# Kernel optimization log

Hardware: AMD Instinct MI355X
Metric: run time of the kernel (lower is better)

Reference implementation:

```python
import jax, jax.numpy as jnp
import numpy as np

D, H, F, E, K = 1024, 16, 2048, 8, 2
EPS = 1e-5


def layernorm(x, g, b):
    m = jnp.mean(x, axis=-1, keepdims=True)
    v = jnp.mean((x - m) ** 2, axis=-1, keepdims=True)
    return (x - m) * jax.lax.rsqrt(v + EPS) * g + b


def mha(q_in, k_in, v_in, wq, wk, wv, bq, bk, bv, wo, bo):
    B, Tq, Dm = q_in.shape
    Tk = k_in.shape[1]
    dh = Dm // H
    q = (q_in @ wq + bq).reshape(B, Tq, H, dh)
    k = (k_in @ wk + bk).reshape(B, Tk, H, dh)
    v = (v_in @ wv + bv).reshape(B, Tk, H, dh)
    scores = jnp.einsum('bqhd,bkhd->bhqk', q, k) / jnp.sqrt(jnp.asarray(dh, q.dtype))
    attn = jax.nn.softmax(scores, axis=-1)
    out = jnp.einsum('bhqk,bkhd->bqhd', attn, v).reshape(B, Tq, Dm)
    return out @ wo + bo


def moe(x, rw, rb, w1, b1, w2, b2):
    B, T, Dm = x.shape
    xt = x.reshape(-1, Dm)                      # [N, D]
    N = xt.shape[0]
    logits = xt @ rw + rb                       # [N, E]
    probs = jax.nn.softmax(logits, axis=-1)
    topv, topi = jax.lax.top_k(probs, K)        # [N, K]
    gates = topv / jnp.sum(topv, axis=-1, keepdims=True)
    dense_gates = jnp.zeros((N, E), x.dtype).at[jnp.arange(N)[:, None], topi].set(gates)
    h = jax.nn.relu(jnp.einsum('td,edf->etf', xt, w1) + b1[:, None, :])  # [E, N, F]
    y = jnp.einsum('etf,efd->etd', h, w2) + b2[:, None, :]               # [E, N, D]
    out = jnp.einsum('te,etd->td', dense_gates, y).reshape(B, T, Dm)
    frac = jnp.mean(jnp.sum(jax.nn.one_hot(topi, E, dtype=x.dtype), axis=1) / K, axis=0)  # [E]
    importance = jnp.mean(probs, axis=0)        # [E]
    lb_loss = E * jnp.sum(frac * importance)
    return out, lb_loss


def forward(tgt, memory,
            sa_wq, sa_wk, sa_wv, sa_bq, sa_bk, sa_bv, sa_wo, sa_bo,
            ca_wq, ca_wk, ca_wv, ca_bq, ca_bk, ca_bv, ca_wo, ca_bo,
            ln1_g, ln1_b, ln2_g, ln2_b, ln3_g, ln3_b,
            rw, rb, w1, b1, w2, b2):
    t2 = mha(tgt, tgt, tgt, sa_wq, sa_wk, sa_wv, sa_bq, sa_bk, sa_bv, sa_wo, sa_bo)
    t = layernorm(tgt + t2, ln1_g, ln1_b)
    t2 = mha(t, memory, memory, ca_wq, ca_wk, ca_wv, ca_bq, ca_bk, ca_bv, ca_wo, ca_bo)
    t = layernorm(t + t2, ln2_g, ln2_b)
    t2, lb = moe(t, rw, rb, w1, b1, w2, b2)
    t = layernorm(t + t2, ln3_g, ln3_b)
    return t, lb


def setup_inputs() -> dict:
    key = jax.random.key(0)
    ks = jax.random.split(key, 24)
    s = 1.0 / np.sqrt(D)
    inp = {
        'tgt': jax.random.normal(ks[0], (4, 512, D), jnp.float32),
        'memory': jax.random.normal(ks[1], (4, 512, D), jnp.float32),
    }
    names = ['sa_wq', 'sa_wk', 'sa_wv', 'sa_wo', 'ca_wq', 'ca_wk', 'ca_wv', 'ca_wo']
    for i, n in enumerate(names):
        inp[n] = jax.random.normal(ks[2 + i], (D, D), jnp.float32) * s
    for n in ['sa_bq', 'sa_bk', 'sa_bv', 'sa_bo', 'ca_bq', 'ca_bk', 'ca_bv', 'ca_bo']:
        inp[n] = jnp.zeros((D,), jnp.float32)
    for n in ['ln1_g', 'ln2_g', 'ln3_g']:
        inp[n] = jnp.ones((D,), jnp.float32)
    for n in ['ln1_b', 'ln2_b', 'ln3_b']:
        inp[n] = jnp.zeros((D,), jnp.float32)
    inp['rw'] = jax.random.normal(ks[10], (D, E), jnp.float32) * s
    inp['rb'] = jnp.zeros((E,), jnp.float32)
    inp['w1'] = jax.random.normal(ks[11], (E, D, F), jnp.float32) * s
    inp['b1'] = jnp.zeros((E, F), jnp.float32)
    inp['w2'] = jax.random.normal(ks[12], (E, F, D), jnp.float32) * (1.0 / np.sqrt(F))
    inp['b2'] = jnp.zeros((E, D), jnp.float32)
    return inp


def reference(tgt, memory,
              sa_wq, sa_wk, sa_wv, sa_bq, sa_bk, sa_bv, sa_wo, sa_bo,
              ca_wq, ca_wk, ca_wv, ca_bq, ca_bk, ca_bv, ca_wo, ca_bo,
              ln1_g, ln1_b, ln2_g, ln2_b, ln3_g, ln3_b,
              rw, rb, w1, b1, w2, b2):
    return forward(tgt, memory,
                   sa_wq, sa_wk, sa_wv, sa_bq, sa_bk, sa_bv, sa_wo, sa_bo,
                   ca_wq, ca_wk, ca_wv, ca_bq, ca_bk, ca_bv, ca_wo, ca_bo,
                   ln1_g, ln1_b, ln2_g, ln2_b, ln3_g, ln3_b,
                   rw, rb, w1, b1, w2, b2)
```

## Files before the change

kernel.cpp:

```cpp
#include <hip/hip_runtime.h>

constexpr int Dm = 1024;
constexpr int NH = 16;
constexpr int Ff = 2048;
constexpr int NE = 8;
constexpr int Bn = 4;
constexpr int Tn = 512;
constexpr int Nt = 2048;

typedef float  f32x4  __attribute__((ext_vector_type(4)));
typedef __bf16 bf16x8 __attribute__((ext_vector_type(8)));
typedef unsigned short u16x8 __attribute__((ext_vector_type(8)));

__device__ inline unsigned short f2bf(float f) {
    unsigned u = __builtin_bit_cast(unsigned, f);
    u += 0x7FFFu + ((u >> 16) & 1u);
    return (unsigned short)(u >> 16);
}
__device__ inline float bf2f(unsigned short h) {
    unsigned u = (unsigned)h << 16;
    return __builtin_bit_cast(float, u);
}
__device__ inline void splitbf(float x, unsigned short& hi, unsigned short& lo) {
    hi = f2bf(x);
    lo = f2bf(x - bf2f(hi));
}
__device__ inline bf16x8 ld_frag(const unsigned short* p) {
    return __builtin_bit_cast(bf16x8, *(const u16x8*)p);
}

template <int SPLIT, int ABF, int CBF>
__global__ __launch_bounds__(256) void gemm_bf16_kernel(
    const void* __restrict__ Ain, int lda,
    const float* __restrict__ W0, const float* __restrict__ W1,
    const float* __restrict__ W2, int ldw, size_t weStride,
    const float* __restrict__ B0, const float* __restrict__ B1,
    const float* __restrict__ B2, size_t beStride,
    void* __restrict__ Cout, int ldc,
    int Mparam, int K,
    const int* __restrict__ lst, int lstStride, const int* __restrict__ cnt,
    int mode, int relu)
{
    __shared__ __align__(16) unsigned short AsH[128 * 40];
    __shared__ __align__(16) unsigned short WsH[128 * 40];
    __shared__ __align__(16) unsigned short AsL[SPLIT ? 128 * 40 : 1];
    __shared__ __align__(16) unsigned short WsL[SPLIT ? 128 * 40 : 1];
    __shared__ int inIdx[128];
    __shared__ int outIdx[128];

    const int e = blockIdx.z;
    const int M = (mode == 0) ? Mparam : cnt[e];
    const int m0 = blockIdx.y * 128;
    if (m0 >= M) return;
    const int n0 = blockIdx.x * 128;
    const int seg = n0 >> 10;
    const float* W = ((seg == 0) ? W0 : (seg == 1) ? W1 : W2) + (size_t)e * weStride;
    const float* bias = ((seg == 0) ? B0 : (seg == 1) ? B1 : B2) + (size_t)e * beStride;
    const int nseg = n0 & 1023;
    const int tid = threadIdx.x;

    if (tid < 128) {
        int g = m0 + tid;
        bool valid = g < M;
        int gi, go;
        if (mode == 0) { gi = valid ? g : (M - 1); go = valid ? g : -1; }
        else {
            int pid = lst[(size_t)e * lstStride + (valid ? g : 0)];
            gi = (mode == 1) ? (pid >> 1) : pid;
            go = valid ? pid : -1;
        }
        inIdx[tid] = gi;
        outIdx[tid] = go;
    }
    __syncthreads();

    const int ar = tid >> 1, ahalf = tid & 1;
    const int bn = (tid & 63) * 2, bko = ((tid >> 6) & 3) * 8;
    const float* aBaseF = ABF ? nullptr
        : ((const float*)Ain + (size_t)inIdx[ar] * lda + ahalf * 16);
    const unsigned short* aBaseB = ABF
        ? ((const unsigned short*)Ain + (size_t)inIdx[ar] * lda + ahalf * 16)
        : nullptr;
    const float* wBase = W + (size_t)bko * ldw + nseg + bn;

    const int lane = tid & 63, wv = tid >> 6;
    const int wy = (wv >> 1) * 64, wx = (wv & 1) * 64;
    const int l15 = lane & 15, quad = lane >> 4;

    f32x4 acc[4][4];
    #pragma unroll
    for (int i = 0; i < 4; ++i)
        #pragma unroll
        for (int j = 0; j < 4; ++j) acc[i][j] = (f32x4)0.f;

    for (int k0 = 0; k0 < K; k0 += 32) {
        if (ABF) {
            const unsigned short* ap = aBaseB + k0;
            *(u16x8*)&AsH[ar * 40 + ahalf * 16]     = *(const u16x8*)(ap);
            *(u16x8*)&AsH[ar * 40 + ahalf * 16 + 8] = *(const u16x8*)(ap + 8);
        } else {
            const float* ap = aBaseF + k0;
            float v[16];
            *(float4*)&v[0]  = *(const float4*)(ap);
            *(float4*)&v[4]  = *(const float4*)(ap + 4);
            *(float4*)&v[8]  = *(const float4*)(ap + 8);
            *(float4*)&v[12] = *(const float4*)(ap + 12);
            u16x8 h0, h1, l0, l1;
            #pragma unroll
            for (int i = 0; i < 8; ++i) {
                unsigned short hh, ll;
                splitbf(v[i], hh, ll); h0[i] = hh; l0[i] = ll;
                splitbf(v[8 + i], hh, ll); h1[i] = hh; l1[i] = ll;
            }
            *(u16x8*)&AsH[ar * 40 + ahalf * 16]     = h0;
            *(u16x8*)&AsH[ar * 40 + ahalf * 16 + 8] = h1;
            if (SPLIT) {
                *(u16x8*)&AsL[ar * 40 + ahalf * 16]     = l0;
                *(u16x8*)&AsL[ar * 40 + ahalf * 16 + 8] = l1;
            }
        }
        {
            const float* wp = wBase + (size_t)k0 * ldw;
            float2 wr[8];
            #pragma unroll
            for (int j = 0; j < 8; ++j) wr[j] = *(const float2*)(wp + (size_t)j * ldw);
            u16x8 h0, h1, l0, l1;
            #pragma unroll
            for (int j = 0; j < 8; ++j) {
                if (SPLIT) {
                    unsigned short hh, ll;
                    splitbf(wr[j].x, hh, ll); h0[j] = hh; l0[j] = ll;
                    splitbf(wr[j].y, hh, ll); h1[j] = hh; l1[j] = ll;
                } else {
                    h0[j] = f2bf(wr[j].x);
                    h1[j] = f2bf(wr[j].y);
                }
            }
            *(u16x8*)&WsH[bn * 40 + bko]       = h0;
            *(u16x8*)&WsH[(bn + 1) * 40 + bko] = h1;
            if (SPLIT) {
                *(u16x8*)&WsL[bn * 40 + bko]       = l0;
                *(u16x8*)&WsL[(bn + 1) * 40 + bko] = l1;
            }
        }
        __syncthreads();
        bf16x8 ah[4], bh[4], al[4], bl[4];
        #pragma unroll
        for (int mi = 0; mi < 4; ++mi)
            ah[mi] = ld_frag(&AsH[(wy + mi * 16 + l15) * 40 + quad * 8]);
        #pragma unroll
        for (int ni = 0; ni < 4; ++ni)
            bh[ni] = ld_frag(&WsH[(wx + ni * 16 + l15) * 40 + quad * 8]);
        if (SPLIT) {
            #pragma unroll
            for (int mi = 0; mi < 4; ++mi)
                al[mi] = ld_frag(&AsL[(wy + mi * 16 + l15) * 40 + quad * 8]);
            #pragma unroll
            for (int ni = 0; ni < 4; ++ni)
                bl[ni] = ld_frag(&WsL[(wx + ni * 16 + l15) * 40 + quad * 8]);
        }
        #pragma unroll
        for (int mi = 0; mi < 4; ++mi)
            #pragma unroll
            for (int ni = 0; ni < 4; ++ni) {
                acc[mi][ni] = __builtin_amdgcn_mfma_f32_16x16x32_bf16(
                    ah[mi], bh[ni], acc[mi][ni], 0, 0, 0);
                if (SPLIT) {
                    acc[mi][ni] = __builtin_amdgcn_mfma_f32_16x16x32_bf16(
                        ah[mi], bl[ni], acc[mi][ni], 0, 0, 0);
                    acc[mi][ni] = __builtin_amdgcn_mfma_f32_16x16x32_bf16(
                        al[mi], bh[ni], acc[mi][ni], 0, 0, 0);
                }
            }
        __syncthreads();
    }

    #pragma unroll
    for (int mi = 0; mi < 4; ++mi) {
        #pragma unroll
        for (int r = 0; r < 4; ++r) {
            int rl = wy + mi * 16 + quad * 4 + r;
            int orow = outIdx[rl];
            if (orow < 0) continue;
            #pragma unroll
            for (int ni = 0; ni < 4; ++ni) {
                int col = n0 + wx + ni * 16 + l15;
                float val = acc[mi][ni][r] + bias[col & 1023];
                if (relu) val = fmaxf(val, 0.f);
                if (CBF)
                    ((unsigned short*)Cout)[(size_t)orow * ldc + col] = f2bf(val);
                else
                    ((float*)Cout)[(size_t)orow * ldc + col] = val;
            }
        }
    }
}

__global__ __launch_bounds__(256) void attn_kernel(
    const float* __restrict__ Qp, int qld,
    const float* __restrict__ Kp, int kld, int kOff,
    const float* __restrict__ Vp, int vld, int vOff,
    float* __restrict__ O)
{
    __shared__ __align__(16) unsigned short KtH[64 * 72], KtL[64 * 72];
    __shared__ __align__(16) unsigned short VtH[64 * 72], VtL[64 * 72];
    __shared__ __align__(16) unsigned short PtH[4][16 * 72], PtL[4][16 * 72];

    const int tid = threadIdx.x, lane = tid & 63, wv = tid >> 6;
    const int quad = lane >> 4, l15 = lane & 15;
    const int b = blockIdx.z, h = blockIdx.y, q0 = blockIdx.x * 64;
    const int bT = b * Tn;

    bf16x8 aqh[2], aql[2];
    {
        const float* qp = Qp + (size_t)(bT + q0 + wv * 16 + l15) * qld + h * 64;
        #pragma unroll
        for (int s = 0; s < 2; ++s) {
            float v[8];
            *(float4*)&v[0] = *(const float4*)(qp + s * 32 + quad * 8);
            *(float4*)&v[4] = *(const float4*)(qp + s * 32 + quad * 8 + 4);
            u16x8 th, tl;
            #pragma unroll
            for (int i = 0; i < 8; ++i) {
                unsigned short hh, ll;
                splitbf(v[i], hh, ll); th[i] = hh; tl[i] = ll;
            }
            aqh[s] = __builtin_bit_cast(bf16x8, th);
            aql[s] = __builtin_bit_cast(bf16x8, tl);
        }
    }

    f32x4 oacc[4];
    #pragma unroll
    for (int i = 0; i < 4; ++i) oacc[i] = (f32x4)0.f;
    float mrow[4] = {-1e30f, -1e30f, -1e30f, -1e30f};
    float lrow[4] = {0.f, 0.f, 0.f, 0.f};

    const int rr = tid >> 2, cc = tid & 3;

    for (int kt0 = 0; kt0 < Tn; kt0 += 64) {
        {
            const float* kr = Kp + (size_t)(bT + kt0 + rr) * kld + kOff + h * 64 + cc * 16;
            float v[16];
            *(float4*)&v[0]  = *(const float4*)(kr);
            *(float4*)&v[4]  = *(const float4*)(kr + 4);
            *(float4*)&v[8]  = *(const float4*)(kr + 8);
            *(float4*)&v[12] = *(const float4*)(kr + 12);
            u16x8 h0, h1, l0, l1;
            #pragma unroll
            for (int i = 0; i < 8; ++i) {
                unsigned short hh, ll;
                splitbf(v[i], hh, ll); h0[i] = hh; l0[i] = ll;
                splitbf(v[8 + i], hh, ll); h1[i] = hh; l1[i] = ll;
            }
            *(u16x8*)&KtH[rr * 72 + cc * 16]     = h0;
            *(u16x8*)&KtH[rr * 72 + cc * 16 + 8] = h1;
            *(u16x8*)&KtL[rr * 72 + cc * 16]     = l0;
            *(u16x8*)&KtL[rr * 72 + cc * 16 + 8] = l1;

            const float* vr = Vp + (size_t)(bT + kt0 + rr) * vld + vOff + h * 64 + cc * 16;
            float fv[16];
            *(float4*)&fv[0]  = *(const float4*)(vr);
            *(float4*)&fv[4]  = *(const float4*)(vr + 4);
            *(float4*)&fv[8]  = *(const float4*)(vr + 8);
            *(float4*)&fv[12] = *(const float4*)(vr + 12);
            #pragma unroll
            for (int i = 0; i < 16; ++i) {
                unsigned short hh, ll;
                splitbf(fv[i], hh, ll);
                VtH[(cc * 16 + i) * 72 + rr] = hh;
                VtL[(cc * 16 + i) * 72 + rr] = ll;
            }
        }
        __syncthreads();

        f32x4 sacc[4];
        #pragma unroll
        for (int nt = 0; nt < 4; ++nt) {
            sacc[nt] = (f32x4)0.f;
            #pragma unroll
            for (int s = 0; s < 2; ++s) {
                bf16x8 bkh = ld_frag(&KtH[(nt * 16 + l15) * 72 + s * 32 + quad * 8]);
                bf16x8 bkl = ld_frag(&KtL[(nt * 16 + l15) * 72 + s * 32 + quad * 8]);
                sacc[nt] = __builtin_amdgcn_mfma_f32_16x16x32_bf16(aqh[s], bkh, sacc[nt], 0, 0, 0);
                sacc[nt] = __builtin_amdgcn_mfma_f32_16x16x32_bf16(aqh[s], bkl, sacc[nt], 0, 0, 0);
                sacc[nt] = __builtin_amdgcn_mfma_f32_16x16x32_bf16(aql[s], bkh, sacc[nt], 0, 0, 0);
            }
        }
        #pragma unroll
        for (int nt = 0; nt < 4; ++nt)
            #pragma unroll
            for (int r = 0; r < 4; ++r) sacc[nt][r] *= 0.125f;

        float alpha[4], mnew[4];
        #pragma unroll
        for (int r = 0; r < 4; ++r) {
            float mx = fmaxf(fmaxf(sacc[0][r], sacc[1][r]), fmaxf(sacc[2][r], sacc[3][r]));
            #pragma unroll
            for (int msk = 1; msk < 16; msk <<= 1) mx = fmaxf(mx, __shfl_xor(mx, msk));
            mnew[r] = fmaxf(mrow[r], mx);
            alpha[r] = __expf(mrow[r] - mnew[r]);
            mrow[r] = mnew[r];
        }
        float rs[4] = {0.f, 0.f, 0.f, 0.f};
        #pragma unroll
        for (int nt = 0; nt < 4; ++nt)
            #pragma unroll
            for (int r = 0; r < 4; ++r) {
                float p = __expf(sacc[nt][r] - mnew[r]);
                sacc[nt][r] = p;
                rs[r] += p;
            }
        #pragma unroll
        for (int r = 0; r < 4; ++r) {
            #pragma unroll
            for (int msk = 1; msk < 16; msk <<= 1) rs[r] += __shfl_xor(rs[r], msk);
            lrow[r] = lrow[r] * alpha[r] + rs[r];
        }
        #pragma unroll
        for (int ni = 0; ni < 4; ++ni)
            #pragma unroll
            for (int r = 0; r < 4; ++r) oacc[ni][r] *= alpha[r];

        #pragma unroll
        for (int nt = 0; nt < 4; ++nt)
            #pragma unroll
            for (int r = 0; r < 4; ++r) {
                unsigned short hh, ll;
                splitbf(sacc[nt][r], hh, ll);
                PtH[wv][(quad * 4 + r) * 72 + nt * 16 + l15] = hh;
                PtL[wv][(quad * 4 + r) * 72 + nt * 16 + l15] = ll;
            }
        asm volatile("s_waitcnt lgkmcnt(0)" ::: "memory");

        #pragma unroll
        for (int s = 0; s < 2; ++s) {
            bf16x8 aph = ld_frag(&PtH[wv][l15 * 72 + s * 32 + quad * 8]);
            bf16x8 apl = ld_frag(&PtL[wv][l15 * 72 + s * 32 + quad * 8]);
            #pragma unroll
            for (int ni = 0; ni < 4; ++ni) {
                bf16x8 bvh = ld_frag(&VtH[(ni * 16 + l15) * 72 + s * 32 + quad * 8]);
                bf16x8 bvl = ld_frag(&VtL[(ni * 16 + l15) * 72 + s * 32 + quad * 8]);
                oacc[ni] = __builtin_amdgcn_mfma_f32_16x16x32_bf16(aph, bvh, oacc[ni], 0, 0, 0);
                oacc[ni] = __builtin_amdgcn_mfma_f32_16x16x32_bf16(aph, bvl, oacc[ni], 0, 0, 0);
                oacc[ni] = __builtin_amdgcn_mfma_f32_16x16x32_bf16(apl, bvh, oacc[ni], 0, 0, 0);
            }
        }
        __syncthreads();
    }

    #pragma unroll
    for (int r = 0; r < 4; ++r) {
        float inv = 1.f / lrow[r];
        int orow = bT + q0 + wv * 16 + quad * 4 + r;
        #pragma unroll
        for (int ni = 0; ni < 4; ++ni) {
            int col = h * 64 + ni * 16 + l15;
            O[(size_t)orow * Dm + col] = oacc[ni][r] * inv;
        }
    }
}

__global__ __launch_bounds__(256) void ln_residual_kernel(
    const float* __restrict__ X, const float* __restrict__ R,
    const float* __restrict__ g, const float* __restrict__ bta,
    float* __restrict__ Out)
{
    __shared__ float red[8];
    const int t = blockIdx.x, tid = threadIdx.x;
    float v[4];
    float s = 0.f;
    #pragma unroll
    for (int i = 0; i < 4; ++i) {
        int c = tid + i * 256;
        v[i] = X[(size_t)t * Dm + c] + R[(size_t)t * Dm + c];
        s += v[i];
    }
    #pragma unroll
    for (int off = 32; off; off >>= 1) s += __shfl_down(s, off);
    const int wid = tid >> 6;
    if ((tid & 63) == 0) red[wid] = s;
    __syncthreads();
    const float mean = (red[0] + red[1] + red[2] + red[3]) * (1.f / 1024.f);
    float s2 = 0.f;
    #pragma unroll
    for (int i = 0; i < 4; ++i) { float d = v[i] - mean; s2 += d * d; }
    #pragma unroll
    for (int off = 32; off; off >>= 1) s2 += __shfl_down(s2, off);
    if ((tid & 63) == 0) red[4 + wid] = s2;
    __syncthreads();
    const float var  = (red[4] + red[5] + red[6] + red[7]) * (1.f / 1024.f);
    const float rstd = rsqrtf(var + 1e-5f);
    #pragma unroll
    for (int i = 0; i < 4; ++i) {
        int c = tid + i * 256;
        Out[(size_t)t * Dm + c] = (v[i] - mean) * rstd * g[c] + bta[c];
    }
}

constexpr int RT_TPB = 32;
__global__ __launch_bounds__(256) void router_kernel(
    const float* __restrict__ X, const float* __restrict__ rw,
    const float* __restrict__ rb, float* __restrict__ gatep,
    int* __restrict__ elist, int* __restrict__ ecnt,
    float* __restrict__ impf, float* __restrict__ cntf)
{
    __shared__ float simp[NE];
    __shared__ int   scnt[NE];
    __shared__ int   sbase[NE];
    __shared__ int   sexp[RT_TPB][2];
    __shared__ int   spos[RT_TPB][2];

    const int tid = threadIdx.x, lane = tid & 63, wv = tid >> 6;
    if (tid < NE) { simp[tid] = 0.f; scnt[tid] = 0; }
    __syncthreads();

    const int t0 = blockIdx.x * RT_TPB;

    for (int i = 0; i < 8; ++i) {
        const int slot = wv * 8 + i;
        const int t = t0 + slot;
        float l[NE];
        #pragma unroll
        for (int e = 0; e < NE; ++e) l[e] = 0.f;
        #pragma unroll
        for (int j = 0; j < Dm / 64; ++j) {
            int d = lane + j * 64;
            float x = X[(size_t)t * Dm + d];
            #pragma unroll
            for (int e = 0; e < NE; ++e) l[e] += x * rw[d * NE + e];
        }
        #pragma unroll
        for (int e = 0; e < NE; ++e) {
            float vv = l[e];
            #pragma unroll
            for (int off = 32; off; off >>= 1) vv += __shfl_down(vv, off);
            l[e] = vv;
        }
        if (lane == 0) {
            float mx = -1e30f;
            #pragma unroll
            for (int e = 0; e < NE; ++e) { l[e] += rb[e]; mx = fmaxf(mx, l[e]); }
            float p[NE];
            float sum = 0.f;
            #pragma unroll
            for (int e = 0; e < NE; ++e) { p[e] = __expf(l[e] - mx); sum += p[e]; }
            const float inv = 1.f / sum;
            int e0 = 0, e1 = 0;
            float v0 = -1.f, v1 = -1.f;
            #pragma unroll
            for (int e = 0; e < NE; ++e) {
                float pe = p[e] * inv;
                atomicAdd(&simp[e], pe);
                if (pe > v0)      { v1 = v0; e1 = e0; v0 = pe; e0 = e; }
                else if (pe > v1) { v1 = pe; e1 = e; }
            }
            const float gs = 1.f / (v0 + v1);
            sexp[slot][0] = e0;
            sexp[slot][1] = e1;
            spos[slot][0] = atomicAdd(&scnt[e0], 1);
            spos[slot][1] = atomicAdd(&scnt[e1], 1);
            gatep[2 * t]     = v0 * gs;
            gatep[2 * t + 1] = v1 * gs;
        }
    }
    __syncthreads();

    if (tid < NE) {
        sbase[tid] = atomicAdd(&ecnt[tid], scnt[tid]);
        atomicAdd(&impf[tid], simp[tid]);
        atomicAdd(&cntf[tid], (float)scnt[tid]);
    }
    __syncthreads();

    if (tid < RT_TPB * 2) {
        const int slot = tid >> 1, k = tid & 1;
        const int e = sexp[slot][k];
        elist[e * Nt + sbase[e] + spos[slot][k]] = 2 * (t0 + slot) + k;
    }
}

__global__ void init_kernel(int* ecnt, float* impf, float* cntf)
{
    int i = threadIdx.x;
    if (i < NE) { ecnt[i] = 0; impf[i] = 0.f; cntf[i] = 0.f; }
}

__global__ void lb_kernel(const float* __restrict__ impf,
                          const float* __restrict__ cntf,
                          float* __restrict__ out)
{
    if (threadIdx.x == 0) {
        float s = 0.f;
        for (int e = 0; e < NE; ++e) s += cntf[e] * impf[e];
        out[0] = (float)NE * s / ((float)Nt * 2.f * (float)Nt);
    }
}

__global__ __launch_bounds__(256) void moe_combine(
    const float* __restrict__ Y, const float* __restrict__ gatep,
    float* __restrict__ Out)
{
    int i = blockIdx.x * 256 + threadIdx.x;
    int t = i >> 10, c = i & 1023;
    Out[i] = gatep[2 * t] * Y[(size_t)(2 * t) * Dm + c]
           + gatep[2 * t + 1] * Y[(size_t)(2 * t + 1) * Dm + c];
}

extern "C" void kernel_launch(void* const* d_in, const int* in_sizes, int n_in,
                              void* d_out, int out_size, void* d_ws, size_t ws_size,
                              hipStream_t stream)
{
    const float* tgt   = (const float*)d_in[0];
    const float* memry = (const float*)d_in[1];
    const float* sa_wq = (const float*)d_in[2];
    const float* sa_wk = (const float*)d_in[3];
    const float* sa_wv = (const float*)d_in[4];
    const float* sa_wo = (const float*)d_in[5];
    const float* ca_wq = (const float*)d_in[6];
    const float* ca_wk = (const float*)d_in[7];
    const float* ca_wv = (const float*)d_in[8];
    const float* ca_wo = (const float*)d_in[9];
    const float* sa_bq = (const float*)d_in[10];
    const float* sa_bk = (const float*)d_in[11];
    const float* sa_bv = (const float*)d_in[12];
    const float* sa_bo = (const float*)d_in[13];
    const float* ca_bq = (const float*)d_in[14];
    const float* ca_bk = (const float*)d_in[15];
    const float* ca_bv = (const float*)d_in[16];
    const float* ca_bo = (const float*)d_in[17];
    const float* ln1_g = (const float*)d_in[18];
    const float* ln2_g = (const float*)d_in[19];
    const float* ln3_g = (const float*)d_in[20];
    const float* ln1_b = (const float*)d_in[21];
    const float* ln2_b = (const float*)d_in[22];
    const float* ln3_b = (const float*)d_in[23];
    const float* rw    = (const float*)d_in[24];
    const float* rb    = (const float*)d_in[25];
    const float* w1    = (const float*)d_in[26];
    const float* b1    = (const float*)d_in[27];
    const float* w2    = (const float*)d_in[28];
    const float* b2    = (const float*)d_in[29];

    float* ws = (float*)d_ws;
    const size_t ND = (size_t)Nt * Dm;
    float* qkv  = ws;
    float* qc   = ws;
    float* kvc  = ws + ND;
    float* attnO = ws + 3 * ND;
    unsigned short* hbuf16 = (unsigned short*)ws;
    float* t2   = ws + 4 * ND;
    float* tb   = ws + 5 * ND;
    float* ybuf = ws + 6 * ND;
    float* gatep = ws + 8 * ND;
    int*   elist = (int*)(gatep + 2 * Nt);
    int*   ecnt  = elist + NE * Nt;
    float* impf  = (float*)(ecnt + NE);
    float* cntf  = impf + NE;
    float* outp  = (float*)d_out;

    dim3 blk(256);
    dim3 attnGrid(Tn / 64, NH, Bn);

    gemm_bf16_kernel<1, 0, 0><<<dim3(24, 16, 1), blk, 0, stream>>>(
        tgt, Dm, sa_wq, sa_wk, sa_wv, Dm, 0, sa_bq, sa_bk, sa_bv, 0,
        qkv, 3 * Dm, Nt, Dm, nullptr, 0, nullptr, 0, 0);
    attn_kernel<<<attnGrid, blk, 0, stream>>>(
        qkv, 3 * Dm, qkv, 3 * Dm, 1024, qkv, 3 * Dm, 2048, attnO);
    gemm_bf16_kernel<1, 0, 0><<<dim3(8, 16, 1), blk, 0, stream>>>(
        attnO, Dm, sa_wo, sa_wo, sa_wo, Dm, 0, sa_bo, sa_bo, sa_bo, 0,
        t2, Dm, Nt, Dm, nullptr, 0, nullptr, 0, 0);
    ln_residual_kernel<<<Nt, blk, 0, stream>>>(tgt, t2, ln1_g, ln1_b, tb);

    gemm_bf16_kernel<1, 0, 0><<<dim3(8, 16, 1), blk, 0, stream>>>(
        tb, Dm, ca_wq, ca_wq, ca_wq, Dm, 0, ca_bq, ca_bq, ca_bq, 0,
        qc, Dm, Nt, Dm, nullptr, 0, nullptr, 0, 0);
    gemm_bf16_kernel<1, 0, 0><<<dim3(16, 16, 1), blk, 0, stream>>>(
        memry, Dm, ca_wk, ca_wv, ca_wv, Dm, 0, ca_bk, ca_bv, ca_bv, 0,
        kvc, 2 * Dm, Nt, Dm, nullptr, 0, nullptr, 0, 0);
    attn_kernel<<<attnGrid, blk, 0, stream>>>(
        qc, Dm, kvc, 2 * Dm, 0, kvc, 2 * Dm, 1024, attnO);
    gemm_bf16_kernel<1, 0, 0><<<dim3(8, 16, 1), blk, 0, stream>>>(
        attnO, Dm, ca_wo, ca_wo, ca_wo, Dm, 0, ca_bo, ca_bo, ca_bo, 0,
        t2, Dm, Nt, Dm, nullptr, 0, nullptr, 0, 0);
    ln_residual_kernel<<<Nt, blk, 0, stream>>>(tb, t2, ln2_g, ln2_b, tb);

    init_kernel<<<1, 64, 0, stream>>>(ecnt, impf, cntf);
    router_kernel<<<Nt / RT_TPB, blk, 0, stream>>>(tb, rw, rb, gatep, elist, ecnt, impf, cntf);
    gemm_bf16_kernel<0, 0, 1><<<dim3(16, 16, 8), blk, 0, stream>>>(
        tb, Dm, w1, w1 + 1024, w1 + 1024, Ff, (size_t)Dm * Ff, b1, b1 + 1024, b1 + 1024, Ff,
        hbuf16, Ff, 0, Dm, elist, Nt, ecnt, 1, 1);
    gemm_bf16_kernel<0, 1, 0><<<dim3(8, 16, 8), blk, 0, stream>>>(
        hbuf16, Ff, w2, w2, w2, Dm, (size_t)Ff * Dm, b2, b2, b2, Dm,
        ybuf, Dm, 0, Ff, elist, Nt, ecnt, 2, 0);
    moe_combine<<<(Nt * Dm) / 256, blk, 0, stream>>>(ybuf, gatep, t2);
    ln_residual_kernel<<<Nt, blk, 0, stream>>>(tb, t2, ln3_g, ln3_b, outp);
    lb_kernel<<<1, 64, 0, stream>>>(impf, cntf, outp + ND);
}
```

Baseline: 830.7 us.

## Fuse cross-attn KV projection into QKV launch, prefetch tiles, fold MoE combine into GEMM

The cross-attention K/V projection of memory is merged into the self-attention QKV GEMM launch through an extra x-range of blocks, so both run in one grid with 40 column tiles. The GEMM and attention kernels now load the next K-tile into registers before doing the MFMA work on the current one, a register double-buffer meant to hide global-load latency. The MoE second GEMM multiplies by the gate and atomically adds straight into t2, which a new zero kernel clears first. This removes the ybuf round trip and the separate combine kernel, at the cost of atomics, non-deterministic summation order and higher register pressure.

```diff
diff --git a/kernel.cpp b/kernel.cpp
--- a/kernel.cpp
+++ b/kernel.cpp
@@ -29,7 +29,7 @@
     return __builtin_bit_cast(bf16x8, *(const u16x8*)p);
 }
 
-template <int SPLIT, int ABF, int CBF>
+template <int SPLIT, int ABF, int CBF, int ACC>
 __global__ __launch_bounds__(256) void gemm_bf16_kernel(
     const void* __restrict__ Ain, int lda,
     const float* __restrict__ W0, const float* __restrict__ W1,
@@ -39,7 +39,12 @@
     void* __restrict__ Cout, int ldc,
     int Mparam, int K,
     const int* __restrict__ lst, int lstStride, const int* __restrict__ cnt,
-    int mode, int relu)
+    int mode, int relu,
+    const void* __restrict__ Ain2, const float* __restrict__ W0b,
+    const float* __restrict__ W1b, const float* __restrict__ B0b,
+    const float* __restrict__ B1b, void* __restrict__ Cout2, int ldc2,
+    int xSplit,
+    const float* __restrict__ gatep, float* __restrict__ accOut)
 {
     __shared__ __align__(16) unsigned short AsH[128 * 40];
     __shared__ __align__(16) unsigned short WsH[128 * 40];
@@ -52,10 +57,21 @@
     const int M = (mode == 0) ? Mparam : cnt[e];
     const int m0 = blockIdx.y * 128;
     if (m0 >= M) return;
-    const int n0 = blockIdx.x * 128;
+
+    int bx = blockIdx.x;
+    const void* Aptr = Ain;
+    void* Cptr = Cout;
+    int myldc = ldc;
+    const float *w0 = W0, *w1 = W1, *w2 = W2, *b0 = B0, *b1 = B1, *b2 = B2;
+    if (xSplit && bx >= xSplit) {
+        bx -= xSplit;
+        Aptr = Ain2; Cptr = Cout2; myldc = ldc2;
+        w0 = W0b; w1 = W1b; w2 = W1b; b0 = B0b; b1 = B1b; b2 = B1b;
+    }
+    const int n0 = bx * 128;
     const int seg = n0 >> 10;
-    const float* W = ((seg == 0) ? W0 : (seg == 1) ? W1 : W2) + (size_t)e * weStride;
-    const float* bias = ((seg == 0) ? B0 : (seg == 1) ? B1 : B2) + (size_t)e * beStride;
+    const float* W = ((seg == 0) ? w0 : (seg == 1) ? w1 : w2) + (size_t)e * weStride;
+    const float* bias = ((seg == 0) ? b0 : (seg == 1) ? b1 : b2) + (size_t)e * beStride;
     const int nseg = n0 & 1023;
     const int tid = threadIdx.x;
 
@@ -77,9 +93,9 @@
     const int ar = tid >> 1, ahalf = tid & 1;
     const int bn = (tid & 63) * 2, bko = ((tid >> 6) & 3) * 8;
     const float* aBaseF = ABF ? nullptr
-        : ((const float*)Ain + (size_t)inIdx[ar] * lda + ahalf * 16);
+        : ((const float*)Aptr + (size_t)inIdx[ar] * lda + ahalf * 16);
     const unsigned short* aBaseB = ABF
-        ? ((const unsigned short*)Ain + (size_t)inIdx[ar] * lda + ahalf * 16)
+        ? ((const unsigned short*)Aptr + (size_t)inIdx[ar] * lda + ahalf * 16)
         : nullptr;
     const float* wBase = W + (size_t)bko * ldw + nseg + bn;
 
@@ -93,24 +109,44 @@
         #pragma unroll
         for (int j = 0; j < 4; ++j) acc[i][j] = (f32x4)0.f;
 
-    for (int k0 = 0; k0 < K; k0 += 32) {
+    float av[16];
+    u16x8 a16[2];
+    float2 wreg[8];
+
+    auto loadA = [&](int k0) {
         if (ABF) {
             const unsigned short* ap = aBaseB + k0;
-            *(u16x8*)&AsH[ar * 40 + ahalf * 16]     = *(const u16x8*)(ap);
-            *(u16x8*)&AsH[ar * 40 + ahalf * 16 + 8] = *(const u16x8*)(ap + 8);
+            a16[0] = *(const u16x8*)(ap);
+            a16[1] = *(const u16x8*)(ap + 8);
         } else {
             const float* ap = aBaseF + k0;
-            float v[16];
-            *(float4*)&v[0]  = *(const float4*)(ap);
-            *(float4*)&v[4]  = *(const float4*)(ap + 4);
-            *(float4*)&v[8]  = *(const float4*)(ap + 8);
-            *(float4*)&v[12] = *(const float4*)(ap + 12);
+            *(float4*)&av[0]  = *(const float4*)(ap);
+            *(float4*)&av[4]  = *(const float4*)(ap + 4);
+            *(float4*)&av[8]  = *(const float4*)(ap + 8);
+            *(float4*)&av[12] = *(const float4*)(ap + 12);
+        }
+    };
+    auto loadW = [&](int k0) {
+        const float* wp = wBase + (size_t)k0 * ldw;
+        #pragma unroll
+        for (int j = 0; j < 8; ++j) wreg[j] = *(const float2*)(wp + (size_t)j * ldw);
+    };
+    auto storeA = [&]() {
+        if (ABF) {
+            *(u16x8*)&AsH[ar * 40 + ahalf * 16]     = a16[0];
+            *(u16x8*)&AsH[ar * 40 + ahalf * 16 + 8] = a16[1];
+        } else {
             u16x8 h0, h1, l0, l1;
             #pragma unroll
             for (int i = 0; i < 8; ++i) {
-                unsigned short hh, ll;
-                splitbf(v[i], hh, ll); h0[i] = hh; l0[i] = ll;
-                splitbf(v[8 + i], hh, ll); h1[i] = hh; l1[i] = ll;
+                if (SPLIT) {
+                    unsigned short hh, ll;
+                    splitbf(av[i], hh, ll); h0[i] = hh; l0[i] = ll;
+                    splitbf(av[8 + i], hh, ll); h1[i] = hh; l1[i] = ll;
+                } else {
+                    h0[i] = f2bf(av[i]);
+                    h1[i] = f2bf(av[8 + i]);
+                }
             }
             *(u16x8*)&AsH[ar * 40 + ahalf * 16]     = h0;
             *(u16x8*)&AsH[ar * 40 + ahalf * 16 + 8] = h1;
@@ -119,31 +155,35 @@
                 *(u16x8*)&AsL[ar * 40 + ahalf * 16 + 8] = l1;
             }
         }
-        {
-            const float* wp = wBase + (size_t)k0 * ldw;
-            float2 wr[8];
-            #pragma unroll
-            for (int j = 0; j < 8; ++j) wr[j] = *(const float2*)(wp + (size_t)j * ldw);
-            u16x8 h0, h1, l0, l1;
-            #pragma unroll
-            for (int j = 0; j < 8; ++j) {
-                if (SPLIT) {
-                    unsigned short hh, ll;
-                    splitbf(wr[j].x, hh, ll); h0[j] = hh; l0[j] = ll;
-                    splitbf(wr[j].y, hh, ll); h1[j] = hh; l1[j] = ll;
-                } else {
-                    h0[j] = f2bf(wr[j].x);
-                    h1[j] = f2bf(wr[j].y);
-                }
-            }
-            *(u16x8*)&WsH[bn * 40 + bko]       = h0;
-            *(u16x8*)&WsH[(bn + 1) * 40 + bko] = h1;
+    };
+    auto storeW = [&]() {
+        u16x8 h0, h1, l0, l1;
+        #pragma unroll
+        for (int j = 0; j < 8; ++j) {
             if (SPLIT) {
-                *(u16x8*)&WsL[bn * 40 + bko]       = l0;
-                *(u16x8*)&WsL[(bn + 1) * 40 + bko] = l1;
-            }
-        }
+                unsigned short hh, ll;
+                splitbf(wreg[j].x, hh, ll); h0[j] = hh; l0[j] = ll;
+                splitbf(wreg[j].y, hh, ll); h1[j] = hh; l1[j] = ll;
+            } else {
+                h0[j] = f2bf(wreg[j].x);
+                h1[j] = f2bf(wreg[j].y);
+            }
+        }
+        *(u16x8*)&WsH[bn * 40 + bko]       = h0;
+        *(u16x8*)&WsH[(bn + 1) * 40 + bko] = h1;
+        if (SPLIT) {
+            *(u16x8*)&WsL[bn * 40 + bko]       = l0;
+            *(u16x8*)&WsL[(bn + 1) * 40 + bko] = l1;
+        }
+    };
+
+    loadA(0);
+    loadW(0);
+    for (int k0 = 0; k0 < K; k0 += 32) {
+        storeA();
+        storeW();
         __syncthreads();
+        if (k0 + 32 < K) { loadA(k0 + 32); loadW(k0 + 32); }
         bf16x8 ah[4], bh[4], al[4], bl[4];
         #pragma unroll
         for (int mi = 0; mi < 4; ++mi)
@@ -187,10 +227,14 @@
                 int col = n0 + wx + ni * 16 + l15;
                 float val = acc[mi][ni][r] + bias[col & 1023];
                 if (relu) val = fmaxf(val, 0.f);
-                if (CBF)
-                    ((unsigned short*)Cout)[(size_t)orow * ldc + col] = f2bf(val);
-                else
-                    ((float*)Cout)[(size_t)orow * ldc + col] = val;
+                if (ACC) {
+                    float g = gatep[orow];
+                    atomicAdd(&accOut[(size_t)(orow >> 1) * Dm + col], g * val);
+                } else if (CBF) {
+                    ((unsigned short*)Cptr)[(size_t)orow * myldc + col] = f2bf(val);
+                } else {
+                    ((float*)Cptr)[(size_t)orow * myldc + col] = val;
+                }
             }
         }
     }
@@ -238,41 +282,45 @@
 
     const int rr = tid >> 2, cc = tid & 3;
 
+    float kf[16], vf[16];
+    auto loadKV = [&](int kt0) {
+        const float* kr = Kp + (size_t)(bT + kt0 + rr) * kld + kOff + h * 64 + cc * 16;
+        *(float4*)&kf[0]  = *(const float4*)(kr);
+        *(float4*)&kf[4]  = *(const float4*)(kr + 4);
+        *(float4*)&kf[8]  = *(const float4*)(kr + 8);
+        *(float4*)&kf[12] = *(const float4*)(kr + 12);
+        const float* vr = Vp + (size_t)(bT + kt0 + rr) * vld + vOff + h * 64 + cc * 16;
+        *(float4*)&vf[0]  = *(const float4*)(vr);
+        *(float4*)&vf[4]  = *(const float4*)(vr + 4);
+        *(float4*)&vf[8]  = *(const float4*)(vr + 8);
+        *(float4*)&vf[12] = *(const float4*)(vr + 12);
+    };
+    auto storeKV = [&]() {
+        u16x8 h0, h1, l0, l1;
+        #pragma unroll
+        for (int i = 0; i < 8; ++i) {
+            unsigned short hh, ll;
+            splitbf(kf[i], hh, ll); h0[i] = hh; l0[i] = ll;
+            splitbf(kf[8 + i], hh, ll); h1[i] = hh; l1[i] = ll;
+        }
+        *(u16x8*)&KtH[rr * 72 + cc * 16]     = h0;
+        *(u16x8*)&KtH[rr * 72 + cc * 16 + 8] = h1;
+        *(u16x8*)&KtL[rr * 72 + cc * 16]     = l0;
+        *(u16x8*)&KtL[rr * 72 + cc * 16 + 8] = l1;
+        #pragma unroll
+        for (int i = 0; i < 16; ++i) {
+            unsigned short hh, ll;
+            splitbf(vf[i], hh, ll);
+            VtH[(cc * 16 + i) * 72 + rr] = hh;
+            VtL[(cc * 16 + i) * 72 + rr] = ll;
+        }
+    };
+
+    loadKV(0);
     for (int kt0 = 0; kt0 < Tn; kt0 += 64) {
-        {
-            const float* kr = Kp + (size_t)(bT + kt0 + rr) * kld + kOff + h * 64 + cc * 16;
-            float v[16];
-            *(float4*)&v[0]  = *(const float4*)(kr);
-            *(float4*)&v[4]  = *(const float4*)(kr + 4);
-            *(float4*)&v[8]  = *(const float4*)(kr + 8);
-            *(float4*)&v[12] = *(const float4*)(kr + 12);
-            u16x8 h0, h1, l0, l1;
-            #pragma unroll
-            for (int i = 0; i < 8; ++i) {
-                unsigned short hh, ll;
-                splitbf(v[i], hh, ll); h0[i] = hh; l0[i] = ll;
-                splitbf(v[8 + i], hh, ll); h1[i] = hh; l1[i] = ll;
-            }
-            *(u16x8*)&KtH[rr * 72 + cc * 16]     = h0;
-            *(u16x8*)&KtH[rr * 72 + cc * 16 + 8] = h1;
-            *(u16x8*)&KtL[rr * 72 + cc * 16]     = l0;
-            *(u16x8*)&KtL[rr * 72 + cc * 16 + 8] = l1;
-
-            const float* vr = Vp + (size_t)(bT + kt0 + rr) * vld + vOff + h * 64 + cc * 16;
-            float fv[16];
-            *(float4*)&fv[0]  = *(const float4*)(vr);
-            *(float4*)&fv[4]  = *(const float4*)(vr + 4);
-            *(float4*)&fv[8]  = *(const float4*)(vr + 8);
-            *(float4*)&fv[12] = *(const float4*)(vr + 12);
-            #pragma unroll
-            for (int i = 0; i < 16; ++i) {
-                unsigned short hh, ll;
-                splitbf(fv[i], hh, ll);
-                VtH[(cc * 16 + i) * 72 + rr] = hh;
-                VtL[(cc * 16 + i) * 72 + rr] = ll;
-            }
-        }
+        storeKV();
         __syncthreads();
+        if (kt0 + 64 < Tn) loadKV(kt0 + 64);
 
         f32x4 sacc[4];
         #pragma unroll
@@ -480,10 +528,17 @@
     }
 }
 
-__global__ void init_kernel(int* ecnt, float* impf, float* cntf)
+__global__ __launch_bounds__(256) void zero_kernel(
+    float* __restrict__ t2, int* __restrict__ ecnt,
+    float* __restrict__ impf, float* __restrict__ cntf)
 {
-    int i = threadIdx.x;
-    if (i < NE) { ecnt[i] = 0; impf[i] = 0.f; cntf[i] = 0.f; }
+    int i = blockIdx.x * 256 + threadIdx.x;
+    *(float4*)&t2[(size_t)i * 4] = make_float4(0.f, 0.f, 0.f, 0.f);
+    if (blockIdx.x == 0 && threadIdx.x < NE) {
+        ecnt[threadIdx.x] = 0;
+        impf[threadIdx.x] = 0.f;
+        cntf[threadIdx.x] = 0.f;
+    }
 }
 
 __global__ void lb_kernel(const float* __restrict__ impf,
@@ -495,16 +550,6 @@
         for (int e = 0; e < NE; ++e) s += cntf[e] * impf[e];
         out[0] = (float)NE * s / ((float)Nt * 2.f * (float)Nt);
     }
-}
-
-__global__ __launch_bounds__(256) void moe_combine(
-    const float* __restrict__ Y, const float* __restrict__ gatep,
-    float* __restrict__ Out)
-{
-    int i = blockIdx.x * 256 + threadIdx.x;
-    int t = i >> 10, c = i & 1023;
-    Out[i] = gatep[2 * t] * Y[(size_t)(2 * t) * Dm + c]
-           + gatep[2 * t + 1] * Y[(size_t)(2 * t + 1) * Dm + c];
 }
 
 extern "C" void kernel_launch(void* const* d_in, const int* in_sizes, int n_in,
@@ -546,12 +591,11 @@
     const size_t ND = (size_t)Nt * Dm;
     float* qkv  = ws;
     float* qc   = ws;
-    float* kvc  = ws + ND;
+    unsigned short* hbuf16 = (unsigned short*)ws;
     float* attnO = ws + 3 * ND;
-    unsigned short* hbuf16 = (unsigned short*)ws;
     float* t2   = ws + 4 * ND;
     float* tb   = ws + 5 * ND;
-    float* ybuf = ws + 6 * ND;
+    float* kvc  = ws + 6 * ND;
     float* gatep = ws + 8 * ND;
     int*   elist = (int*)(gatep + 2 * Nt);
     int*   ecnt  = elist + NE * Nt;
@@ -562,38 +606,46 @@
     dim3 blk(256);
     dim3 attnGrid(Tn / 64, NH, Bn);
 
-    gemm_bf16_kernel<1, 0, 0><<<dim3(24, 16, 1), blk, 0, stream>>>(
+    gemm_bf16_kernel<1, 0, 0, 0><<<dim3(40, 16, 1), blk, 0, stream>>>(
         tgt, Dm, sa_wq, sa_wk, sa_wv, Dm, 0, sa_bq, sa_bk, sa_bv, 0,
-        qkv, 3 * Dm, Nt, Dm, nullptr, 0, nullptr, 0, 0);
+        qkv, 3 * Dm, Nt, Dm, nullptr, 0, nullptr, 0, 0,
+        memry, ca_wk, ca_wv, ca_bk, ca_bv, kvc, 2 * Dm, 24,
+        nullptr, nullptr);
     attn_kernel<<<attnGrid, blk, 0, stream>>>(
         qkv, 3 * Dm, qkv, 3 * Dm, 1024, qkv, 3 * Dm, 2048, attnO);
-    gemm_bf16_kernel<1, 0, 0><<<dim3(8, 16, 1), blk, 0, stream>>>(
+    gemm_bf16_kernel<1, 0, 0, 0><<<dim3(8, 16, 1), blk, 0, stream>>>(
         attnO, Dm, sa_wo, sa_wo, sa_wo, Dm, 0, sa_bo, sa_bo, sa_bo, 0,
-        t2, Dm, Nt, Dm, nullptr, 0, nullptr, 0, 0);
+        t2, Dm, Nt, Dm, nullptr, 0, nullptr, 0, 0,
+        nullptr, nullptr, nullptr, nullptr, nullptr, nullptr, 0, 0,
+        nullptr, nullptr);
     ln_residual_kernel<<<Nt, blk, 0, stream>>>(tgt, t2, ln1_g, ln1_b, tb);
 
-    gemm_bf16_kernel<1, 0, 0><<<dim3(8, 16, 1), blk, 0, stream>>>(
+    gemm_bf16_kernel<1, 0, 0, 0><<<dim3(8, 16, 1), blk, 0, stream>>>(
         tb, Dm, ca_wq, ca_wq, ca_wq, Dm, 0, ca_bq, ca_bq, ca_bq, 0,
-        qc, Dm, Nt, Dm, nullptr, 0, nullptr, 0, 0);
-    gemm_bf16_kernel<1, 0, 0><<<dim3(16, 16, 1), blk, 0, stream>>>(
-        memry, Dm, ca_wk, ca_wv, ca_wv, Dm, 0, ca_bk, ca_bv, ca_bv, 0,
-        kvc, 2 * Dm, Nt, Dm, nullptr, 0, nullptr, 0, 0);
+        qc, Dm, Nt, Dm, nullptr, 0, nullptr, 0, 0,
+        nullptr, nullptr, nullptr, nullptr, nullptr, nullptr, 0, 0,
+        nullptr, nullptr);
     attn_kernel<<<attnGrid, blk, 0, stream>>>(
         qc, Dm, kvc, 2 * Dm, 0, kvc, 2 * Dm, 1024, attnO);
-    gemm_bf16_kernel<1, 0, 0><<<dim3(8, 16, 1), blk, 0, stream>>>(
+    gemm_bf16_kernel<1, 0, 0, 0><<<dim3(8, 16, 1), blk, 0, stream>>>(
         attnO, Dm, ca_wo, ca_wo, ca_wo, Dm, 0, ca_bo, ca_bo, ca_bo, 0,
-        t2, Dm, Nt, Dm, nullptr, 0, nullptr, 0, 0);
+        t2, Dm, Nt, Dm, nullptr, 0, nullptr, 0, 0,
+        nullptr, nullptr, nullptr, nullptr, nullptr, nullptr, 0, 0,
+        nullptr, nullptr);
     ln_residual_kernel<<<Nt, blk, 0, stream>>>(tb, t2, ln2_g, ln2_b, tb);
 
-    init_kernel<<<1, 64, 0, stream>>>(ecnt, impf, cntf);
+    zero_kernel<<<(Nt * Dm) / 1024, blk, 0, stream>>>(t2, ecnt, impf, cntf);
     router_kernel<<<Nt / RT_TPB, blk, 0, stream>>>(tb, rw, rb, gatep, elist, ecnt, impf, cntf);
-    gemm_bf16_kernel<0, 0, 1><<<dim3(16, 16, 8), blk, 0, stream>>>(
+    gemm_bf16_kernel<0, 0, 1, 0><<<dim3(16, 16, 8), blk, 0, stream>>>(
         tb, Dm, w1, w1 + 1024, w1 + 1024, Ff, (size_t)Dm * Ff, b1, b1 + 1024, b1 + 1024, Ff,
-        hbuf16, Ff, 0, Dm, elist, Nt, ecnt, 1, 1);
-    gemm_bf16_kernel<0, 1, 0><<<dim3(8, 16, 8), blk, 0, stream>>>(
+        hbuf16, Ff, 0, Dm, elist, Nt, ecnt, 1, 1,
+        nullptr, nullptr, nullptr, nullptr, nullptr, nullptr, 0, 0,
+        nullptr, nullptr);
+    gemm_bf16_kernel<0, 1, 0, 1><<<dim3(8, 16, 8), blk, 0, stream>>>(
         hbuf16, Ff, w2, w2, w2, Dm, (size_t)Ff * Dm, b2, b2, b2, Dm,
-        ybuf, Dm, 0, Ff, elist, Nt, ecnt, 2, 0);
-    moe_combine<<<(Nt * Dm) / 256, blk, 0, stream>>>(ybuf, gatep, t2);
+        nullptr, Dm, 0, Ff, elist, Nt, ecnt, 2, 0,
+        nullptr, nullptr, nullptr, nullptr, nullptr, nullptr, 0, 0,
+        gatep, t2);
     ln_residual_kernel<<<Nt, blk, 0, stream>>>(tb, t2, ln3_g, ln3_b, outp);
     lb_kernel<<<1, 64, 0, stream>>>(impf, cntf, outp + ND);
 }
```

Result: no change. 819.6 us (-1.3%).
